# Kernel tuning notes

Measured on AMD Instinct MI355X. Metric: run time of the kernel, lower is better.

## Reference

```python
import jax, jax.numpy as jnp
import numpy as np

Q, N, K, D, H = 1000, 50000, 5, 16, 256
B, S = 4096, 512
IN = D + 1 + D + (K - 1)  # update-network input dim = 37
ABILITY_SCALE = 1.0


def setup_inputs() -> dict:
    key = jax.random.key(0)
    ks = jax.random.split(key, 12)
    theta_embed = jax.random.normal(ks[0], (N + 1, D), dtype=jnp.float32).at[0].set(0.0)
    alpha_raw = 0.1 * jax.random.normal(ks[1], (Q + 1, D), dtype=jnp.float32)
    beta_base = 0.05 * jax.random.normal(ks[2], (Q + 1, 1), dtype=jnp.float32)
    beta_gaps = jnp.full((Q + 1, K - 2), 0.3, dtype=jnp.float32)
    W_h = 0.01 * jax.random.normal(ks[3], (IN, H), dtype=jnp.float32)
    b_h = jnp.zeros((H,), jnp.float32)
    W_g = 0.01 * jax.random.normal(ks[4], (H, D), dtype=jnp.float32)
    b_g = jnp.full((D,), -2.0, jnp.float32)
    W_d = 0.01 * jax.random.normal(ks[5], (H, D), dtype=jnp.float32)
    b_d = jnp.zeros((D,), jnp.float32)
    student_ids = jax.random.randint(ks[6], (B, S), 0, N)
    questions = jax.random.randint(ks[7], (B, S), 0, Q)
    responses = jax.random.randint(ks[8], (B, S), 0, K)
    return dict(theta_embed=theta_embed, alpha_raw=alpha_raw, beta_base=beta_base,
                beta_gaps=beta_gaps, W_h=W_h, b_h=b_h, W_g=W_g, b_g=b_g,
                W_d=W_d, b_d=b_d, student_ids=student_ids, questions=questions,
                responses=responses)


def reference(theta_embed, alpha_raw, beta_base, beta_gaps, W_h, b_h, W_g, b_g,
              W_d, b_d, student_ids, questions, responses):
    cat_vals = jnp.arange(K, dtype=jnp.float32)
    # Item params for all (B, S) positions at once.
    alpha = jnp.exp(0.3 * alpha_raw[questions])                       # (B,S,D)
    sp_gaps = jax.nn.softplus(beta_gaps[questions])                   # (B,S,K-2)
    zero = jnp.zeros(questions.shape + (1,), jnp.float32)
    beta = beta_base[questions] + jnp.concatenate([zero, jnp.cumsum(sp_gaps, -1)], -1)  # (B,S,K-1)

    theta0 = theta_embed[student_ids[:, 0]] * ABILITY_SCALE           # (B,D)

    def step(theta, inp):
        a_t, b_t, r_t = inp                                           # (B,D),(B,K-1),(B,)
        z = jnp.sum(a_t * theta, axis=-1, keepdims=True)              # (B,1)
        logits = jnp.concatenate([jnp.zeros_like(z), jnp.cumsum(z - b_t, -1)], -1)  # (B,K)
        probs = jax.nn.softmax(logits, axis=-1)
        expected = probs @ cat_vals                                   # (B,)
        surprise = r_t - expected
        u = jnp.concatenate([theta, surprise[:, None], a_t, b_t], -1)  # (B,IN)
        h = jnp.tanh(u @ W_h + b_h)
        gate = jax.nn.sigmoid(h @ W_g + b_g)
        delta = jnp.tanh(h @ W_d + b_d)
        return theta + gate * delta, (theta, logits, probs)

    xs = (alpha.transpose(1, 0, 2), beta.transpose(1, 0, 2),
          responses.T.astype(jnp.float32))
    _, (thetas, logits, probs) = jax.lax.scan(step, theta0, xs)
    theta_out = thetas.transpose(1, 0, 2)                             # (B,S,D)
    logits = logits.transpose(1, 0, 2)                                # (B,S,K)
    probs = probs.transpose(1, 0, 2)                                  # (B,S,K)
    return theta_out, alpha, beta, logits, probs
```

## Files before the change

### kernel.cpp

```cpp
#include <hip/hip_runtime.h>
#include <cstddef>
#include <cstdint>


namespace {
constexpr int Bn = 4096;
constexpr int Sn = 512;
constexpr int Qn = 1000;

typedef __attribute__((ext_vector_type(8))) __bf16 bf16x8;
typedef __attribute__((ext_vector_type(4))) float f32x4;
typedef __attribute__((ext_vector_type(4))) unsigned short u16x4;

__device__ __forceinline__ float frcp(float x) { return __builtin_amdgcn_rcpf(x); }
__device__ __forceinline__ float ftanh(float x) {
  return 1.0f - 2.0f * frcp(__expf(2.0f * x) + 1.0f);
}
__device__ __forceinline__ float fsigmoid(float x) {
  return frcp(1.0f + __expf(-x));
}
__device__ __forceinline__ float fsoftplus(float x) {
  return (x > 20.0f) ? x : log1pf(__expf(x));
}
__device__ __forceinline__ unsigned short f2b(float x) {
  return __builtin_bit_cast(unsigned short, (__bf16)x);
}
__device__ __forceinline__ int permk(int k) {
  if (k < 16) return k;
  if (k < 32) return k + 1;
  if (k == 32) return 16;
  return k;
}

#define WAVE_FENCE() asm volatile("s_waitcnt lgkmcnt(0)" ::: "memory")
#define USWZ(s_, off_) ((((s_) * 128) + (off_)) ^ (((s_) & 7) << 4))
#define HSWZ(s_, off_) ((((s_) * 512) + (off_)) ^ (((s_) & 7) << 4))

__global__ void precompute_kernel(const float* __restrict__ alpha_raw,
                                  const float* __restrict__ beta_base,
                                  const float* __restrict__ beta_gaps,
                                  float* __restrict__ alpha_q,
                                  float* __restrict__ beta_q) {
  int tid = blockIdx.x * 256 + threadIdx.x;
  if (tid < (Qn + 1) * 16) alpha_q[tid] = __expf(0.3f * alpha_raw[tid]);
  if (tid < Qn + 1) {
    float base = beta_base[tid];
    float sp0 = fsoftplus(beta_gaps[tid * 3 + 0]);
    float sp1 = fsoftplus(beta_gaps[tid * 3 + 1]);
    float sp2 = fsoftplus(beta_gaps[tid * 3 + 2]);
    beta_q[tid * 4 + 0] = base;
    beta_q[tid * 4 + 1] = base + sp0;
    beta_q[tid * 4 + 2] = base + sp0 + sp1;
    beta_q[tid * 4 + 3] = base + sp0 + sp1 + sp2;
  }
}

__global__ void itemout_kernel(const int* __restrict__ questions,
                               const float4* __restrict__ alpha_q4,
                               const float4* __restrict__ beta_q4,
                               float4* __restrict__ out_alpha4,
                               float4* __restrict__ out_beta4) {
  int tid = blockIdx.x * 256 + threadIdx.x;
  int pos = tid >> 2, j = tid & 3;
  if (pos >= Bn * Sn) return;
  int q = questions[pos];
  out_alpha4[(size_t)pos * 4 + j] = alpha_q4[(size_t)q * 4 + j];
  if (j == 0) out_beta4[pos] = beta_q4[q];
}

__global__ __launch_bounds__(256, 1) void scan_kernel(
    const float* __restrict__ theta_embed,
    const float* __restrict__ W_h, const float* __restrict__ b_h,
    const float* __restrict__ W_g, const float* __restrict__ b_g,
    const float* __restrict__ W_d, const float* __restrict__ b_d,
    const int* __restrict__ student_ids, const int* __restrict__ questions,
    const int* __restrict__ responses,
    const float* __restrict__ alpha_q, const float4* __restrict__ beta_q4,
    float* __restrict__ out_theta, float* __restrict__ out_logits,
    float* __restrict__ out_probs) {
  __shared__ char sU[4 * 2048];
  __shared__ char sH[2 * 8192];

  const int tid = threadIdx.x;
  const int lane = tid & 63;
  const int wv = tid >> 6;
  const int s = lane & 15;
  const int g = lane >> 4;
  const int bs = blockIdx.x * 16 + s;

  char* uB = sU + wv * 2048;
  {
    int4 zz = {0, 0, 0, 0};
    ((int4*)uB)[lane * 2] = zz;
    ((int4*)uB)[lane * 2 + 1] = zz;
  }

  bf16x8 whA[4][2];
#pragma unroll
  for (int m = 0; m < 4; ++m) {
    const int j = 64 * wv + 16 * m + s;
#pragma unroll
    for (int kk = 0; kk < 2; ++kk) {
#pragma unroll
      for (int e = 0; e < 8; ++e) {
        const int k = kk * 32 + g * 8 + e;
        float v = 0.0f;
        if (k < 37) v = W_h[permk(k) * 256 + j];
        whA[m][kk][e] = (__bf16)v;
      }
    }
  }
  bf16x8 wgdA[2][8];
#pragma unroll
  for (int m = 0; m < 2; ++m) {
    const float* Wm = m ? W_d : W_g;
#pragma unroll
    for (int kk = 0; kk < 8; ++kk) {
#pragma unroll
      for (int e = 0; e < 8; ++e) {
        const int k = kk * 32 + g * 8 + e;
        wgdA[m][kk][e] = (__bf16)Wm[k * 16 + s];
      }
    }
  }
  f32x4 bias_h[4];
#pragma unroll
  for (int m = 0; m < 4; ++m)
    bias_h[m] = *(const f32x4*)(b_h + 64 * wv + 16 * m + 4 * g);
  const f32x4 bias_g = *(const f32x4*)(b_g + 4 * g);
  const f32x4 bias_d = *(const f32x4*)(b_d + 4 * g);

  const int* qrow = questions + (size_t)bs * Sn;
  const int* rrow = responses + (size_t)bs * Sn;

  f32x4 th = *(const f32x4*)(theta_embed +
                             (size_t)student_ids[(size_t)bs * Sn] * 16 + 4 * g);

  int r = rrow[0];
  int q0 = qrow[0];
  float4 a4 = *(const float4*)(alpha_q + (size_t)q0 * 16 + 4 * g);
  float4 bq = beta_q4[q0];
  int qn = qrow[1], rn = rrow[1];

  for (int t = 0; t < Sn; ++t) {
    const float4 a4n = *(const float4*)(alpha_q + (size_t)qn * 16 + 4 * g);
    const float4 bqn = beta_q4[qn];
    const int t2 = (t + 2 < Sn) ? t + 2 : Sn - 1;
    const int qn2 = qrow[t2];
    const int rn2 = rrow[t2];

    float zp = a4.x * th.x + a4.y * th.y + a4.z * th.z + a4.w * th.w;
    zp += __shfl_xor(zp, 16);
    zp += __shfl_xor(zp, 32);
    const float z = zp;

    const float l1 = z - bq.x;
    const float l2 = l1 + z - bq.y;
    const float l3 = l2 + z - bq.z;
    const float l4 = l3 + z - bq.w;
    const float m = fmaxf(fmaxf(fmaxf(l1, l2), fmaxf(l3, l4)), 0.0f);
    const float e0 = __expf(-m);
    const float e1 = __expf(l1 - m);
    const float e2 = __expf(l2 - m);
    const float e3 = __expf(l3 - m);
    const float e4 = __expf(l4 - m);
    const float inv = frcp(e0 + e1 + e2 + e3 + e4);
    const float expected = (e1 + 2.0f * e2 + 3.0f * e3 + 4.0f * e4) * inv;
    const float surprise = (float)r - expected;

    if (wv == (t & 3)) {
      const size_t pos = (size_t)bs * Sn + t;
      *(f32x4*)(out_theta + pos * 16 + 4 * g) = th;
      const float lv = (g == 0) ? 0.0f : (g == 1) ? l1 : (g == 2) ? l2 : l3;
      const float pv = ((g == 0) ? e0 : (g == 1) ? e1 : (g == 2) ? e2 : e3) * inv;
      out_logits[pos * 5 + g] = lv;
      out_probs[pos * 5 + g] = pv;
      if (g == 3) {
        out_logits[pos * 5 + 4] = l4;
        out_probs[pos * 5 + 4] = e4 * inv;
      }
    }

    {
      u16x4 thb = {f2b(th.x), f2b(th.y), f2b(th.z), f2b(th.w)};
      *(u16x4*)(uB + USWZ(s, 8 * g)) = thb;
      u16x4 ab = {f2b(a4.x), f2b(a4.y), f2b(a4.z), f2b(a4.w)};
      *(u16x4*)(uB + USWZ(s, 32 + 8 * g)) = ab;
      if (g == 0) {
        u16x4 sb = {f2b(surprise), f2b(bq.x), f2b(bq.y), f2b(bq.z)};
        *(u16x4*)(uB + USWZ(s, 64)) = sb;
        *(unsigned short*)(uB + USWZ(s, 72)) = f2b(bq.w);
      }
    }
    WAVE_FENCE();

    const bf16x8 ub0 = *(const bf16x8*)(uB + USWZ(s, 16 * g));
    const bf16x8 ub1 = *(const bf16x8*)(uB + USWZ(s, 64 + 16 * g));
    f32x4 acc0 = bias_h[0], acc1 = bias_h[1], acc2 = bias_h[2], acc3 = bias_h[3];
    acc0 = __builtin_amdgcn_mfma_f32_16x16x32_bf16(whA[0][0], ub0, acc0, 0, 0, 0);
    acc1 = __builtin_amdgcn_mfma_f32_16x16x32_bf16(whA[1][0], ub0, acc1, 0, 0, 0);
    acc2 = __builtin_amdgcn_mfma_f32_16x16x32_bf16(whA[2][0], ub0, acc2, 0, 0, 0);
    acc3 = __builtin_amdgcn_mfma_f32_16x16x32_bf16(whA[3][0], ub0, acc3, 0, 0, 0);
    acc0 = __builtin_amdgcn_mfma_f32_16x16x32_bf16(whA[0][1], ub1, acc0, 0, 0, 0);
    acc1 = __builtin_amdgcn_mfma_f32_16x16x32_bf16(whA[1][1], ub1, acc1, 0, 0, 0);
    acc2 = __builtin_amdgcn_mfma_f32_16x16x32_bf16(whA[2][1], ub1, acc2, 0, 0, 0);
    acc3 = __builtin_amdgcn_mfma_f32_16x16x32_bf16(whA[3][1], ub1, acc3, 0, 0, 0);

    char* hB = sH + (t & 1) * 8192;
    {
      u16x4 h0 = {f2b(ftanh(acc0.x)), f2b(ftanh(acc0.y)), f2b(ftanh(acc0.z)), f2b(ftanh(acc0.w))};
      *(u16x4*)(hB + HSWZ(s, 128 * wv + 8 * g)) = h0;
      u16x4 h1 = {f2b(ftanh(acc1.x)), f2b(ftanh(acc1.y)), f2b(ftanh(acc1.z)), f2b(ftanh(acc1.w))};
      *(u16x4*)(hB + HSWZ(s, 128 * wv + 32 + 8 * g)) = h1;
      u16x4 h2 = {f2b(ftanh(acc2.x)), f2b(ftanh(acc2.y)), f2b(ftanh(acc2.z)), f2b(ftanh(acc2.w))};
      *(u16x4*)(hB + HSWZ(s, 128 * wv + 64 + 8 * g)) = h2;
      u16x4 h3 = {f2b(ftanh(acc3.x)), f2b(ftanh(acc3.y)), f2b(ftanh(acc3.z)), f2b(ftanh(acc3.w))};
      *(u16x4*)(hB + HSWZ(s, 128 * wv + 96 + 8 * g)) = h3;
    }
    __syncthreads();

    f32x4 ag = bias_g, ad = bias_d;
#pragma unroll
    for (int kk = 0; kk < 8; ++kk) {
      const bf16x8 hb = *(const bf16x8*)(hB + HSWZ(s, 64 * kk + 16 * g));
      ag = __builtin_amdgcn_mfma_f32_16x16x32_bf16(wgdA[0][kk], hb, ag, 0, 0, 0);
      ad = __builtin_amdgcn_mfma_f32_16x16x32_bf16(wgdA[1][kk], hb, ad, 0, 0, 0);
    }
    th.x += fsigmoid(ag.x) * ftanh(ad.x);
    th.y += fsigmoid(ag.y) * ftanh(ad.y);
    th.z += fsigmoid(ag.z) * ftanh(ad.z);
    th.w += fsigmoid(ag.w) * ftanh(ad.w);

    a4 = a4n; bq = bqn; r = rn;
    qn = qn2; rn = rn2;
  }
}

}

extern "C" void kernel_launch(void* const* d_in, const int* in_sizes, int n_in,
                              void* d_out, int out_size, void* d_ws, size_t ws_size,
                              hipStream_t stream) {
  const float* theta_embed = (const float*)d_in[0];
  const float* alpha_raw   = (const float*)d_in[1];
  const float* beta_base   = (const float*)d_in[2];
  const float* beta_gaps   = (const float*)d_in[3];
  const float* W_h = (const float*)d_in[4];
  const float* b_h = (const float*)d_in[5];
  const float* W_g = (const float*)d_in[6];
  const float* b_g = (const float*)d_in[7];
  const float* W_d = (const float*)d_in[8];
  const float* b_d = (const float*)d_in[9];
  const int* student_ids = (const int*)d_in[10];
  const int* questions   = (const int*)d_in[11];
  const int* responses   = (const int*)d_in[12];

  float* out = (float*)d_out;
  float* out_theta  = out;
  float* out_alpha  = out_theta + (size_t)Bn * Sn * 16;
  float* out_beta   = out_alpha + (size_t)Bn * Sn * 16;
  float* out_logits = out_beta  + (size_t)Bn * Sn * 4;
  float* out_probs  = out_logits + (size_t)Bn * Sn * 5;

  float* alpha_q = (float*)d_ws;
  float* beta_q  = alpha_q + (size_t)(Qn + 1) * 16;

  hipLaunchKernelGGL(precompute_kernel, dim3(63), dim3(256), 0, stream,
                     alpha_raw, beta_base, beta_gaps, alpha_q, beta_q);
  hipLaunchKernelGGL(itemout_kernel, dim3((Bn * Sn * 4) / 256), dim3(256), 0, stream,
                     questions, (const float4*)alpha_q, (const float4*)beta_q,
                     (float4*)out_alpha, (float4*)out_beta);
  hipLaunchKernelGGL(scan_kernel, dim3(Bn / 16), dim3(256), 0, stream,
                     theta_embed, W_h, b_h, W_g, b_g, W_d, b_d,
                     student_ids, questions, responses,
                     alpha_q, (const float4*)beta_q,
                     out_theta, out_logits, out_probs);
}
```

Measured before the change: 610.4 us.

## Use padded LDS strides, raw v_exp, split MFMA chains and lighter barrier

Replaces the XOR-swizzled LDS layout with padded row strides (144/528 bytes), uses v_exp_f32 directly with log2e scaling instead of __expf, and splits the gate/delta MFMA accumulation into two independent chains to shorten the dependency chain. It also swaps __syncthreads for an explicit waitcnt plus s_barrier and unrolls the time loop by two. The goal is to cut latency on the serial per-step critical path, at the cost of more LDS and registers and a small change in rounding.

```diff
diff --git a/kernel.cpp b/kernel.cpp
--- a/kernel.cpp
+++ b/kernel.cpp
@@ -8,16 +8,24 @@
 constexpr int Sn = 512;
 constexpr int Qn = 1000;
 
+constexpr int UST = 144;
+constexpr int HST = 528;
+
 typedef __attribute__((ext_vector_type(8))) __bf16 bf16x8;
 typedef __attribute__((ext_vector_type(4))) float f32x4;
 typedef __attribute__((ext_vector_type(4))) unsigned short u16x4;
 
 __device__ __forceinline__ float frcp(float x) { return __builtin_amdgcn_rcpf(x); }
+__device__ __forceinline__ float fexp2(float x) {
+  float r;
+  asm("v_exp_f32 %0, %1" : "=v"(r) : "v"(x));
+  return r;
+}
 __device__ __forceinline__ float ftanh(float x) {
-  return 1.0f - 2.0f * frcp(__expf(2.0f * x) + 1.0f);
+  return 1.0f - 2.0f * frcp(fexp2(x * 2.88539008177793f) + 1.0f);
 }
 __device__ __forceinline__ float fsigmoid(float x) {
-  return frcp(1.0f + __expf(-x));
+  return frcp(1.0f + fexp2(x * -1.44269504088896f));
 }
 __device__ __forceinline__ float fsoftplus(float x) {
   return (x > 20.0f) ? x : log1pf(__expf(x));
@@ -33,8 +41,12 @@
 }
 
 #define WAVE_FENCE() asm volatile("s_waitcnt lgkmcnt(0)" ::: "memory")
-#define USWZ(s_, off_) ((((s_) * 128) + (off_)) ^ (((s_) & 7) << 4))
-#define HSWZ(s_, off_) ((((s_) * 512) + (off_)) ^ (((s_) & 7) << 4))
+#define BLOCK_SYNC()                                        \
+  do {                                                      \
+    asm volatile("s_waitcnt lgkmcnt(0)" ::: "memory");      \
+    __builtin_amdgcn_s_barrier();                           \
+    asm volatile("" ::: "memory");                          \
+  } while (0)
 
 __global__ void precompute_kernel(const float* __restrict__ alpha_raw,
                                   const float* __restrict__ beta_base,
@@ -78,8 +90,8 @@
     const float* __restrict__ alpha_q, const float4* __restrict__ beta_q4,
     float* __restrict__ out_theta, float* __restrict__ out_logits,
     float* __restrict__ out_probs) {
-  __shared__ char sU[4 * 2048];
-  __shared__ char sH[2 * 8192];
+  __shared__ char sU[4 * 16 * UST];
+  __shared__ char sH[2 * 16 * HST];
 
   const int tid = threadIdx.x;
   const int lane = tid & 63;
@@ -88,11 +100,12 @@
   const int g = lane >> 4;
   const int bs = blockIdx.x * 16 + s;
 
-  char* uB = sU + wv * 2048;
+  char* uB = sU + wv * (16 * UST);
   {
     int4 zz = {0, 0, 0, 0};
-    ((int4*)uB)[lane * 2] = zz;
-    ((int4*)uB)[lane * 2 + 1] = zz;
+    char* p = uB + (lane >> 2) * UST + (lane & 3) * 32;
+    *(int4*)p = zz;
+    *(int4*)(p + 16) = zz;
   }
 
   bf16x8 whA[4][2];
@@ -129,6 +142,7 @@
     bias_h[m] = *(const f32x4*)(b_h + 64 * wv + 16 * m + 4 * g);
   const f32x4 bias_g = *(const f32x4*)(b_g + 4 * g);
   const f32x4 bias_d = *(const f32x4*)(b_d + 4 * g);
+  const f32x4 zero4 = {0.0f, 0.0f, 0.0f, 0.0f};
 
   const int* qrow = questions + (size_t)bs * Sn;
   const int* rrow = responses + (size_t)bs * Sn;
@@ -142,6 +156,7 @@
   float4 bq = beta_q4[q0];
   int qn = qrow[1], rn = rrow[1];
 
+#pragma unroll 2
   for (int t = 0; t < Sn; ++t) {
     const float4 a4n = *(const float4*)(alpha_q + (size_t)qn * 16 + 4 * g);
     const float4 bqn = beta_q4[qn];
@@ -159,11 +174,11 @@
     const float l3 = l2 + z - bq.z;
     const float l4 = l3 + z - bq.w;
     const float m = fmaxf(fmaxf(fmaxf(l1, l2), fmaxf(l3, l4)), 0.0f);
-    const float e0 = __expf(-m);
-    const float e1 = __expf(l1 - m);
-    const float e2 = __expf(l2 - m);
-    const float e3 = __expf(l3 - m);
-    const float e4 = __expf(l4 - m);
+    const float e0 = fexp2(-m * 1.44269504088896f);
+    const float e1 = fexp2((l1 - m) * 1.44269504088896f);
+    const float e2 = fexp2((l2 - m) * 1.44269504088896f);
+    const float e3 = fexp2((l3 - m) * 1.44269504088896f);
+    const float e4 = fexp2((l4 - m) * 1.44269504088896f);
     const float inv = frcp(e0 + e1 + e2 + e3 + e4);
     const float expected = (e1 + 2.0f * e2 + 3.0f * e3 + 4.0f * e4) * inv;
     const float surprise = (float)r - expected;
@@ -182,50 +197,60 @@
     }
 
     {
+      char* ur = uB + s * UST;
       u16x4 thb = {f2b(th.x), f2b(th.y), f2b(th.z), f2b(th.w)};
-      *(u16x4*)(uB + USWZ(s, 8 * g)) = thb;
+      *(u16x4*)(ur + 8 * g) = thb;
       u16x4 ab = {f2b(a4.x), f2b(a4.y), f2b(a4.z), f2b(a4.w)};
-      *(u16x4*)(uB + USWZ(s, 32 + 8 * g)) = ab;
+      *(u16x4*)(ur + 32 + 8 * g) = ab;
       if (g == 0) {
         u16x4 sb = {f2b(surprise), f2b(bq.x), f2b(bq.y), f2b(bq.z)};
-        *(u16x4*)(uB + USWZ(s, 64)) = sb;
-        *(unsigned short*)(uB + USWZ(s, 72)) = f2b(bq.w);
+        *(u16x4*)(ur + 64) = sb;
+        *(unsigned short*)(ur + 72) = f2b(bq.w);
       }
     }
     WAVE_FENCE();
 
-    const bf16x8 ub0 = *(const bf16x8*)(uB + USWZ(s, 16 * g));
-    const bf16x8 ub1 = *(const bf16x8*)(uB + USWZ(s, 64 + 16 * g));
-    f32x4 acc0 = bias_h[0], acc1 = bias_h[1], acc2 = bias_h[2], acc3 = bias_h[3];
-    acc0 = __builtin_amdgcn_mfma_f32_16x16x32_bf16(whA[0][0], ub0, acc0, 0, 0, 0);
-    acc1 = __builtin_amdgcn_mfma_f32_16x16x32_bf16(whA[1][0], ub0, acc1, 0, 0, 0);
-    acc2 = __builtin_amdgcn_mfma_f32_16x16x32_bf16(whA[2][0], ub0, acc2, 0, 0, 0);
-    acc3 = __builtin_amdgcn_mfma_f32_16x16x32_bf16(whA[3][0], ub0, acc3, 0, 0, 0);
+    const bf16x8 ub0 = *(const bf16x8*)(uB + s * UST + 16 * g);
+    const bf16x8 ub1 = *(const bf16x8*)(uB + s * UST + 64 + 16 * g);
+    f32x4 acc0 = __builtin_amdgcn_mfma_f32_16x16x32_bf16(whA[0][0], ub0, bias_h[0], 0, 0, 0);
+    f32x4 acc1 = __builtin_amdgcn_mfma_f32_16x16x32_bf16(whA[1][0], ub0, bias_h[1], 0, 0, 0);
+    f32x4 acc2 = __builtin_amdgcn_mfma_f32_16x16x32_bf16(whA[2][0], ub0, bias_h[2], 0, 0, 0);
+    f32x4 acc3 = __builtin_amdgcn_mfma_f32_16x16x32_bf16(whA[3][0], ub0, bias_h[3], 0, 0, 0);
     acc0 = __builtin_amdgcn_mfma_f32_16x16x32_bf16(whA[0][1], ub1, acc0, 0, 0, 0);
     acc1 = __builtin_amdgcn_mfma_f32_16x16x32_bf16(whA[1][1], ub1, acc1, 0, 0, 0);
     acc2 = __builtin_amdgcn_mfma_f32_16x16x32_bf16(whA[2][1], ub1, acc2, 0, 0, 0);
     acc3 = __builtin_amdgcn_mfma_f32_16x16x32_bf16(whA[3][1], ub1, acc3, 0, 0, 0);
 
-    char* hB = sH + (t & 1) * 8192;
+    char* hB = sH + (t & 1) * (16 * HST);
     {
+      char* hr = hB + s * HST + 128 * wv + 8 * g;
       u16x4 h0 = {f2b(ftanh(acc0.x)), f2b(ftanh(acc0.y)), f2b(ftanh(acc0.z)), f2b(ftanh(acc0.w))};
-      *(u16x4*)(hB + HSWZ(s, 128 * wv + 8 * g)) = h0;
+      *(u16x4*)(hr) = h0;
       u16x4 h1 = {f2b(ftanh(acc1.x)), f2b(ftanh(acc1.y)), f2b(ftanh(acc1.z)), f2b(ftanh(acc1.w))};
-      *(u16x4*)(hB + HSWZ(s, 128 * wv + 32 + 8 * g)) = h1;
+      *(u16x4*)(hr + 32) = h1;
       u16x4 h2 = {f2b(ftanh(acc2.x)), f2b(ftanh(acc2.y)), f2b(ftanh(acc2.z)), f2b(ftanh(acc2.w))};
-      *(u16x4*)(hB + HSWZ(s, 128 * wv + 64 + 8 * g)) = h2;
+      *(u16x4*)(hr + 64) = h2;
       u16x4 h3 = {f2b(ftanh(acc3.x)), f2b(ftanh(acc3.y)), f2b(ftanh(acc3.z)), f2b(ftanh(acc3.w))};
-      *(u16x4*)(hB + HSWZ(s, 128 * wv + 96 + 8 * g)) = h3;
-    }
-    __syncthreads();
-
-    f32x4 ag = bias_g, ad = bias_d;
-#pragma unroll
-    for (int kk = 0; kk < 8; ++kk) {
-      const bf16x8 hb = *(const bf16x8*)(hB + HSWZ(s, 64 * kk + 16 * g));
-      ag = __builtin_amdgcn_mfma_f32_16x16x32_bf16(wgdA[0][kk], hb, ag, 0, 0, 0);
-      ad = __builtin_amdgcn_mfma_f32_16x16x32_bf16(wgdA[1][kk], hb, ad, 0, 0, 0);
-    }
+      *(u16x4*)(hr + 96) = h3;
+    }
+    BLOCK_SYNC();
+
+    const char* hr = hB + s * HST + 16 * g;
+    f32x4 ag0 = bias_g, ad0 = bias_d, ag1 = zero4, ad1 = zero4;
+#pragma unroll
+    for (int kk = 0; kk < 4; ++kk) {
+      const bf16x8 hb = *(const bf16x8*)(hr + 64 * kk);
+      ag0 = __builtin_amdgcn_mfma_f32_16x16x32_bf16(wgdA[0][kk], hb, ag0, 0, 0, 0);
+      ad0 = __builtin_amdgcn_mfma_f32_16x16x32_bf16(wgdA[1][kk], hb, ad0, 0, 0, 0);
+    }
+#pragma unroll
+    for (int kk = 4; kk < 8; ++kk) {
+      const bf16x8 hb = *(const bf16x8*)(hr + 64 * kk);
+      ag1 = __builtin_amdgcn_mfma_f32_16x16x32_bf16(wgdA[0][kk], hb, ag1, 0, 0, 0);
+      ad1 = __builtin_amdgcn_mfma_f32_16x16x32_bf16(wgdA[1][kk], hb, ad1, 0, 0, 0);
+    }
+    const f32x4 ag = ag0 + ag1;
+    const f32x4 ad = ad0 + ad1;
     th.x += fsigmoid(ag.x) * ftanh(ad.x);
     th.y += fsigmoid(ag.y) * ftanh(ad.y);
     th.z += fsigmoid(ag.z) * ftanh(ad.z);
```

Result: no change. 608.3 us (median of 2 runs) (-0.4%).
